# Optimization experiments

Hardware: AMD Instinct MI355X
Metric: run time of the kernel (lower is better)

## Reference

```python
import jax, jax.numpy as jnp
import numpy as np

N_NODES = 500_000
N_EDGES = 8_000_000
N_GRAPHS = 512
N_FEATURES = 128
HIDDEN = 128
N_FILT = 8
OUT_DIM = 64
BN_EPS = 1e-5


def setup_inputs() -> dict:
    key = jax.random.key(0)
    ks = jax.random.split(key, 16)
    rn = lambda k, shape, s=0.05: jax.random.normal(k, shape, jnp.float32) * s
    return {
        "x": jax.random.normal(ks[0], (N_NODES, N_FEATURES), jnp.float32),
        "W1": rn(ks[1], (N_FEATURES, HIDDEN)),
        "b1": jnp.zeros((HIDDEN,), jnp.float32),
        "W2": rn(ks[2], (HIDDEN, N_FILT)),
        "b2": jnp.zeros((N_FILT,), jnp.float32),
        "W0": rn(ks[3], (2 * N_FILT, OUT_DIM)),
        "b0": jnp.zeros((OUT_DIM,), jnp.float32),
        "g1W": rn(ks[4], (OUT_DIM, OUT_DIM)),
        "g1b": jnp.zeros((OUT_DIM,), jnp.float32),
        "l1W": rn(ks[5], (OUT_DIM, OUT_DIM)),
        "g2W": rn(ks[6], (OUT_DIM, N_FEATURES)),
        "g2b": jnp.zeros((N_FEATURES,), jnp.float32),
        "l2W": rn(ks[7], (OUT_DIM, N_FEATURES)),
        "bn_gamma": jnp.ones((N_FEATURES,), jnp.float32),
        "bn_beta": jnp.zeros((N_FEATURES,), jnp.float32),
        "edge_index": jax.random.randint(ks[8], (2, N_EDGES), 0, N_NODES),
        "batch": jnp.sort(jax.random.randint(ks[9], (N_NODES,), 0, N_GRAPHS)),
        "death_edge_idx": jax.random.randint(ks[10], (N_NODES,), 0, N_EDGES),
    }


def _deepset(x, batch, GW, Gb, LW):
    # scatter-mean over graphs, Linear (no bias), gather-broadcast subtract
    sums = jax.ops.segment_sum(x, batch, num_segments=N_GRAPHS)  # [G, d]
    cnt = jax.ops.segment_sum(jnp.ones((x.shape[0], 1), x.dtype), batch,
                              num_segments=N_GRAPHS)             # [G, 1]
    xm = (sums / jnp.maximum(cnt, 1.0)) @ LW                      # Lambda
    return x @ GW + Gb - xm[batch]                                # Gamma - gather


def reference(x, W1, b1, W2, b2, W0, b0, g1W, g1b, l1W, g2W, g2b, l2W,
              bn_gamma, bn_beta, edge_index, batch, death_edge_idx):
    # filtrations MLP: [N, F] -> [N, n_filtrations]
    filtered_v = jax.nn.relu(x @ W1 + b1) @ W2 + b2
    # edge filtration = max of endpoint values (gather + max), [E, n_filtrations]
    filtered_e = jnp.maximum(filtered_v[edge_index[0]], filtered_v[edge_index[1]])
    # persistence pairs (lower-star 0-dim generators): birth = vertex value,
    # death = paired edge value; layout [N, n_filt, 2] -> [N, 2*n_filt]
    births = filtered_v
    deaths = filtered_e[death_edge_idx]
    x0 = jnp.stack([births, deaths], axis=-1).reshape(x.shape[0], 2 * N_FILT)
    # set_fn: Linear -> ReLU -> DeepSet -> ReLU -> DeepSet
    x0 = jax.nn.relu(x0 @ W0 + b0)
    x0 = jax.nn.relu(_deepset(x0, batch, g1W, g1b, l1W))
    x0 = _deepset(x0, batch, g2W, g2b, l2W)
    # residual: x + BatchNorm1d(relu(x0)) with batch statistics
    h = jax.nn.relu(x0)
    mu = h.mean(axis=0)
    var = h.var(axis=0)
    hn = (h - mu) * jax.lax.rsqrt(var + BN_EPS)
    return x + hn * bn_gamma + bn_beta
```

## Files before the change

kernel.cpp:

```cpp
#include <hip/hip_runtime.h>
#include <hip/hip_bf16.h>

#define NNODES 500000
#define NEDGES 8000000
#define NGRAPHS 512
#define NFEAT 128
#define NHID 128
#define NFILT 8
#define ODIM 64
#define BN_EPS 1e-5f
#define NBLK2 3907
#define NBLK3 7813
#define NBLK4 977

typedef __attribute__((ext_vector_type(8))) short bf16x8;
typedef __attribute__((ext_vector_type(4))) float f32x4;
#define MFMA16(a, b, c) __builtin_amdgcn_mfma_f32_16x16x32_bf16(a, b, c, 0, 0, 0)

__device__ inline ushort f2bs(float f) {
  union { __hip_bfloat16 h; ushort u; } cv;
  cv.h = __float2bfloat16(f);
  return cv.u;
}

__global__ void k_pack(const float* __restrict__ g1W, const float* __restrict__ g2W,
                       const float* __restrict__ W1, const float* __restrict__ W0,
                       const int* __restrict__ batch,
                       ushort* __restrict__ pW1, ushort* __restrict__ pW2,
                       ushort* __restrict__ pW0, ushort* __restrict__ pW0p,
                       int* __restrict__ cnt) {
  int idx = blockIdx.x * 256 + threadIdx.x;
  if (idx < 4096) {
    int j = idx & 7, l = (idx >> 3) & 63, kb = (idx >> 9) & 1, ncb = idx >> 10;
    int k = kb * 32 + (l >> 4) * 8 + j, c = ncb * 16 + (l & 15);
    pW1[idx] = f2bs(g1W[k * 64 + c]);
  }
  if (idx < 8192) {
    int j = idx & 7, l = (idx >> 3) & 63, kb = (idx >> 9) & 1, ncb = idx >> 10;
    int k = kb * 32 + (l >> 4) * 8 + j, c = ncb * 16 + (l & 15);
    pW2[idx] = f2bs(g2W[k * 128 + c]);
  }
  if (idx < 16384) {
    int j = idx & 7, l = (idx >> 3) & 63, kb = (idx >> 9) & 3, ncb = idx >> 11;
    int k = kb * 32 + (l >> 4) * 8 + j, c = ncb * 16 + (l & 15);
    pW0[idx] = f2bs(W1[k * 128 + c]);
  }
  if (idx < 4096) {
    int j = idx & 7, l = (idx >> 3) & 63, ncb = idx >> 9;
    int k = (l >> 4) * 8 + j, c = ncb * 16 + (l & 15);
    pW0p[idx] = (k < 16) ? f2bs(W0[k * 64 + c]) : (ushort)0;
  }
  if (idx < NGRAPHS) {
    int g = idx;
    int lo0 = 0, hi0 = NNODES;
    while (lo0 < hi0) { int mid = (lo0 + hi0) >> 1; if (batch[mid] < g) lo0 = mid + 1; else hi0 = mid; }
    int lo1 = lo0, hi1 = NNODES;
    while (lo1 < hi1) { int mid = (lo1 + hi1) >> 1; if (batch[mid] < g + 1) lo1 = mid + 1; else hi1 = mid; }
    cnt[g] = lo1 - lo0;
  }
}

__global__ __launch_bounds__(256) void k_filt(
    const float* __restrict__ x, const ushort* __restrict__ pW0,
    const float* __restrict__ b1, const float* __restrict__ W2,
    const float* __restrict__ b2, ushort* __restrict__ fv16) {
  __shared__ float w2s[128 * 12];
  const int t = threadIdx.x;
  for (int i = t; i < 1024; i += 256) {
    int c = i >> 3, f = i & 7;
    w2s[c * 12 + f] = W2[i];
  }
  __syncthreads();
  const int wv = t >> 6, l = t & 63;
  const int lr = l & 15, lg = l >> 4;
  const int n0 = blockIdx.x * 128 + wv * 32;
  if (n0 >= NNODES) return;

  union { uint4 u; bf16x8 b; } bf[2][4];
#pragma unroll
  for (int mt = 0; mt < 2; ++mt)
#pragma unroll
    for (int kb = 0; kb < 4; ++kb) {
      const float* src = &x[(size_t)(n0 + mt * 16 + lr) * 128 + kb * 32 + lg * 8];
      float v[8];
      *(float4*)&v[0] = *(const float4*)src;
      *(float4*)&v[4] = *(const float4*)(src + 4);
      ushort s[8];
#pragma unroll
      for (int e = 0; e < 8; ++e) s[e] = f2bs(v[e]);
      bf[mt][kb].u = *(uint4*)s;
    }

  float pf0[8], pf1[8];
#pragma unroll
  for (int f = 0; f < 8; ++f) { pf0[f] = 0.f; pf1[f] = 0.f; }

#pragma unroll
  for (int ncb = 0; ncb < 8; ++ncb) {
    union { uint4 u; bf16x8 b; } af[4];
#pragma unroll
    for (int kb = 0; kb < 4; ++kb)
      af[kb].u = *(const uint4*)&pW0[((ncb * 4 + kb) * 64 + l) * 8];
    f32x4 a0 = (f32x4){0.f, 0.f, 0.f, 0.f};
    f32x4 a1 = (f32x4){0.f, 0.f, 0.f, 0.f};
#pragma unroll
    for (int kb = 0; kb < 4; ++kb) {
      a0 = MFMA16(af[kb].b, bf[0][kb].b, a0);
      a1 = MFMA16(af[kb].b, bf[1][kb].b, a1);
    }
    float bbv[4];
    *(float4*)bbv = *(const float4*)&b1[ncb * 16 + lg * 4];
#pragma unroll
    for (int r = 0; r < 4; ++r) {
      const int c = ncb * 16 + lg * 4 + r;
      float h0 = fmaxf(a0[r] + bbv[r], 0.f);
      float h1 = fmaxf(a1[r] + bbv[r], 0.f);
      float w20[4], w21[4];
      *(float4*)w20 = *(const float4*)&w2s[c * 12];
      *(float4*)w21 = *(const float4*)&w2s[c * 12 + 4];
#pragma unroll
      for (int f = 0; f < 4; ++f) {
        pf0[f]     = fmaf(h0, w20[f], pf0[f]);
        pf0[f + 4] = fmaf(h0, w21[f], pf0[f + 4]);
        pf1[f]     = fmaf(h1, w20[f], pf1[f]);
        pf1[f + 4] = fmaf(h1, w21[f], pf1[f + 4]);
      }
    }
  }
#pragma unroll
  for (int f = 0; f < 8; ++f) {
    pf0[f] += __shfl_xor(pf0[f], 16); pf0[f] += __shfl_xor(pf0[f], 32);
    pf1[f] += __shfl_xor(pf1[f], 16); pf1[f] += __shfl_xor(pf1[f], 32);
  }
  if (lg == 0) {
    ushort s0[8], s1[8];
#pragma unroll
    for (int f = 0; f < 8; ++f) {
      float bb = b2[f];
      s0[f] = f2bs(pf0[f] + bb);
      s1[f] = f2bs(pf1[f] + bb);
    }
    *(uint4*)&fv16[(size_t)(n0 + lr) * 8]      = *(uint4*)s0;
    *(uint4*)&fv16[(size_t)(n0 + 16 + lr) * 8] = *(uint4*)s1;
  }
}

__global__ __launch_bounds__(256) void k_pairs(
    const ushort* __restrict__ fv16, const int* __restrict__ edge_index,
    const int* __restrict__ didx, const int* __restrict__ batch,
    const ushort* __restrict__ pW0p, const float* __restrict__ b0,
    ushort* __restrict__ y, float* __restrict__ sums1) {
  __shared__ float ps[4][64];
  __shared__ int pg[4];
  const int t = threadIdx.x, wv = t >> 6, l = t & 63;
  const int lr = l & 15, lg = l >> 4, c0 = lg * 4;
  const int nbase = blockIdx.x * 512;

  union { uint4 u; bf16x8 b; } af[4];
#pragma unroll
  for (int ncb = 0; ncb < 4; ++ncb)
    af[ncb].u = *(const uint4*)&pW0p[(ncb * 64 + l) * 8];

  for (int tile = 0; tile < 4; ++tile) {
    const int n0 = nbase + tile * 128 + wv * 32;
    if (n0 < NNODES) {
      union { uint4 u; bf16x8 b; } bf[2];
      int gN[2];
#pragma unroll
      for (int mt = 0; mt < 2; ++mt) {
        const int n = n0 + mt * 16 + lr;
        gN[mt] = batch[n];
        bf[mt].u = make_uint4(0u, 0u, 0u, 0u);
        if (lg < 2) {
          const int de = didx[n];
          const int u = edge_index[de];
          const int v = edge_index[NEDGES + de];
          ushort4 bb = *(const ushort4*)&fv16[(size_t)n * 8 + lg * 4];
          ushort4 ub = *(const ushort4*)&fv16[(size_t)u * 8 + lg * 4];
          ushort4 vb = *(const ushort4*)&fv16[(size_t)v * 8 + lg * 4];
          const ushort* bp = (const ushort*)&bb;
          const ushort* up = (const ushort*)&ub;
          const ushort* vp = (const ushort*)&vb;
          ushort s[8];
#pragma unroll
          for (int j = 0; j < 4; ++j) {
            s[2 * j] = bp[j];
            float uf = __uint_as_float((unsigned)up[j] << 16);
            float vf = __uint_as_float((unsigned)vp[j] << 16);
            s[2 * j + 1] = (uf > vf) ? up[j] : vp[j];
          }
          bf[mt].u = *(uint4*)s;
        }
      }

      f32x4 acc[2][4];
#pragma unroll
      for (int mt = 0; mt < 2; ++mt)
#pragma unroll
        for (int ncb = 0; ncb < 4; ++ncb) {
          acc[mt][ncb] = (f32x4){0.f, 0.f, 0.f, 0.f};
          acc[mt][ncb] = MFMA16(af[ncb].b, bf[mt].b, acc[mt][ncb]);
        }

      const int g_first = __shfl(gN[0], 0);
      float wsum[4][4];
#pragma unroll
      for (int ncb = 0; ncb < 4; ++ncb)
#pragma unroll
        for (int r = 0; r < 4; ++r) wsum[ncb][r] = 0.f;

#pragma unroll
      for (int mt = 0; mt < 2; ++mt) {
        const int n = n0 + mt * 16 + lr;
        const int g = gN[mt];
        const bool prim = (g == g_first);
#pragma unroll
        for (int ncb = 0; ncb < 4; ++ncb) {
          const int c = ncb * 16 + c0;
          float bbv[4];
          *(float4*)bbv = *(const float4*)&b0[c];
          ushort st[4];
#pragma unroll
          for (int r = 0; r < 4; ++r) {
            float v = fmaxf(acc[mt][ncb][r] + bbv[r], 0.f);
            st[r] = f2bs(v);
            if (prim) wsum[ncb][r] += v;
            else atomicAdd(&sums1[g * 64 + c + r], v);
          }
          *(ushort4*)&y[(size_t)n * 64 + c] = *(ushort4*)st;
        }
      }
#pragma unroll
      for (int ncb = 0; ncb < 4; ++ncb)
#pragma unroll
        for (int r = 0; r < 4; ++r) {
          float w = wsum[ncb][r];
          w += __shfl_xor(w, 1); w += __shfl_xor(w, 2);
          w += __shfl_xor(w, 4); w += __shfl_xor(w, 8);
          if (lr == 0) ps[wv][ncb * 16 + c0 + r] = w;
        }
      if (l == 0) pg[wv] = g_first;
    } else {
      ps[wv][l] = 0.f;
      if (l == 0) pg[wv] = -1;
    }
    __syncthreads();

    if (t < 64) {
      const int bg = pg[0];
      float s = 0.f;
#pragma unroll
      for (int w = 0; w < 4; ++w) {
        const int gv = pg[w];
        if (gv < 0) continue;
        if (gv == bg) s += ps[w][t];
        else atomicAdd(&sums1[gv * 64 + t], ps[w][t]);
      }
      if (bg >= 0) atomicAdd(&sums1[bg * 64 + t], s);
    }
    __syncthreads();
  }
}

template <int D>
__global__ void k_meanlin(const float* __restrict__ sums,
                          const int* __restrict__ cnt,
                          const float* __restrict__ LW,
                          float* __restrict__ xm) {
  __shared__ float m[64];
  const int g = blockIdx.x, t = threadIdx.x;
  const float c = fmaxf((float)cnt[g], 1.f);
  if (t < 64) m[t] = sums[g * 64 + t] / c;
  __syncthreads();
  float a = 0.f;
#pragma unroll
  for (int k = 0; k < 64; ++k) a = fmaf(m[k], LW[k * D + t], a);
  xm[g * D + t] = a;
}

__global__ __launch_bounds__(256) void k_ds1(
    const ushort* __restrict__ ybf, const int* __restrict__ batch,
    const ushort* __restrict__ pW1, const float* __restrict__ g1b,
    const float* __restrict__ xm1, ushort* __restrict__ y2,
    float* __restrict__ sums2) {
  __shared__ float ps[4][64];
  __shared__ int pg[4];
  const int t = threadIdx.x, wv = t >> 6, l = t & 63;
  const int lr = l & 15, lg = l >> 4, c0 = lg * 4;
  const int nbase = blockIdx.x * 512;

  union { uint4 u; bf16x8 b; } af[4][2];
#pragma unroll
  for (int ncb = 0; ncb < 4; ++ncb)
#pragma unroll
    for (int kb = 0; kb < 2; ++kb)
      af[ncb][kb].u = *(const uint4*)&pW1[((ncb * 2 + kb) * 64 + l) * 8];

  for (int tile = 0; tile < 4; ++tile) {
    const int n0 = nbase + tile * 128 + wv * 32;
    if (n0 < NNODES) {
      union { uint4 u; bf16x8 b; } bf[2][2];
#pragma unroll
      for (int mt = 0; mt < 2; ++mt)
#pragma unroll
        for (int kb = 0; kb < 2; ++kb)
          bf[mt][kb].u = *(const uint4*)&ybf[(size_t)(n0 + mt * 16 + lr) * 64 + kb * 32 + lg * 8];

      f32x4 acc[2][4];
#pragma unroll
      for (int mt = 0; mt < 2; ++mt)
#pragma unroll
        for (int ncb = 0; ncb < 4; ++ncb) {
          acc[mt][ncb] = (f32x4){0.f, 0.f, 0.f, 0.f};
          acc[mt][ncb] = MFMA16(af[ncb][0].b, bf[mt][0].b, acc[mt][ncb]);
          acc[mt][ncb] = MFMA16(af[ncb][1].b, bf[mt][1].b, acc[mt][ncb]);
        }

      const int g0 = batch[n0 + lr], g1 = batch[n0 + 16 + lr];
      const int g_first = __shfl(g0, 0);

      float wsum[4][4];
#pragma unroll
      for (int ncb = 0; ncb < 4; ++ncb)
#pragma unroll
        for (int r = 0; r < 4; ++r) wsum[ncb][r] = 0.f;

#pragma unroll
      for (int mt = 0; mt < 2; ++mt) {
        const int n = n0 + mt * 16 + lr;
        const int g = mt ? g1 : g0;
        const bool prim = (g == g_first);
#pragma unroll
        for (int ncb = 0; ncb < 4; ++ncb) {
          const int c = ncb * 16 + c0;
          float xmv[4], bbv[4];
          *(float4*)xmv = *(const float4*)&xm1[g * 64 + c];
          *(float4*)bbv = *(const float4*)&g1b[c];
          ushort st[4];
#pragma unroll
          for (int r = 0; r < 4; ++r) {
            float v = fmaxf(acc[mt][ncb][r] + bbv[r] - xmv[r], 0.f);
            st[r] = f2bs(v);
            if (prim) wsum[ncb][r] += v;
            else atomicAdd(&sums2[g * 64 + c + r], v);
          }
          *(ushort4*)&y2[(size_t)n * 64 + c] = *(ushort4*)st;
        }
      }
#pragma unroll
      for (int ncb = 0; ncb < 4; ++ncb)
#pragma unroll
        for (int r = 0; r < 4; ++r) {
          float w = wsum[ncb][r];
          w += __shfl_xor(w, 1); w += __shfl_xor(w, 2);
          w += __shfl_xor(w, 4); w += __shfl_xor(w, 8);
          if (lr == 0) ps[wv][ncb * 16 + c0 + r] = w;
        }
      if (l == 0) pg[wv] = g_first;
    } else {
      ps[wv][l] = 0.f;
      if (l == 0) pg[wv] = -1;
    }
    __syncthreads();

    if (t < 64) {
      const int bg = pg[0];
      float s = 0.f;
#pragma unroll
      for (int w = 0; w < 4; ++w) {
        const int gv = pg[w];
        if (gv < 0) continue;
        if (gv == bg) s += ps[w][t];
        else atomicAdd(&sums2[gv * 64 + t], ps[w][t]);
      }
      if (bg >= 0) atomicAdd(&sums2[bg * 64 + t], s);
    }
    __syncthreads();
  }
}

__global__ __launch_bounds__(256) void k_ds2a(
    const ushort* __restrict__ y2, const int* __restrict__ batch,
    const ushort* __restrict__ pW2, const float* __restrict__ g2b,
    const float* __restrict__ xm2,
    float* __restrict__ pmu, float* __restrict__ psq) {
  __shared__ float ps[4][128], pq[4][128];
  const int t = threadIdx.x, wv = t >> 6, l = t & 63;
  const int lr = l & 15, lg = l >> 4, c0 = lg * 4;
  const int nbase = blockIdx.x * 512;

  float sw[8][4], sq[8][4];
#pragma unroll
  for (int ncb = 0; ncb < 8; ++ncb)
#pragma unroll
    for (int r = 0; r < 4; ++r) { sw[ncb][r] = 0.f; sq[ncb][r] = 0.f; }

  for (int tile = 0; tile < 4; ++tile) {
    const int n0 = nbase + tile * 128 + wv * 32;
    if (n0 >= NNODES) continue;

    union { uint4 u; bf16x8 b; } bf[2][2];
#pragma unroll
    for (int mt = 0; mt < 2; ++mt)
#pragma unroll
      for (int kb = 0; kb < 2; ++kb)
        bf[mt][kb].u = *(const uint4*)&y2[(size_t)(n0 + mt * 16 + lr) * 64 + kb * 32 + lg * 8];

    const int g0 = batch[n0 + lr], g1 = batch[n0 + 16 + lr];

#pragma unroll
    for (int ncb = 0; ncb < 8; ++ncb) {
      union { uint4 u; bf16x8 b; } af0, af1;
      af0.u = *(const uint4*)&pW2[((ncb * 2 + 0) * 64 + l) * 8];
      af1.u = *(const uint4*)&pW2[((ncb * 2 + 1) * 64 + l) * 8];
      f32x4 a0 = (f32x4){0.f, 0.f, 0.f, 0.f}, a1 = (f32x4){0.f, 0.f, 0.f, 0.f};
      a0 = MFMA16(af0.b, bf[0][0].b, a0); a0 = MFMA16(af1.b, bf[0][1].b, a0);
      a1 = MFMA16(af0.b, bf[1][0].b, a1); a1 = MFMA16(af1.b, bf[1][1].b, a1);

      const int c = ncb * 16 + c0;
      float xm0[4], xm1v[4], bbv[4];
      *(float4*)xm0 = *(const float4*)&xm2[g0 * 128 + c];
      *(float4*)xm1v = *(const float4*)&xm2[g1 * 128 + c];
      *(float4*)bbv = *(const float4*)&g2b[c];
#pragma unroll
      for (int r = 0; r < 4; ++r) {
        float v0 = fmaxf(a0[r] + bbv[r] - xm0[r], 0.f);
        float v1 = fmaxf(a1[r] + bbv[r] - xm1v[r], 0.f);
        sw[ncb][r] += v0 + v1;
        sq[ncb][r] = fmaf(v0, v0, fmaf(v1, v1, sq[ncb][r]));
      }
    }
  }

#pragma unroll
  for (int ncb = 0; ncb < 8; ++ncb)
#pragma unroll
    for (int r = 0; r < 4; ++r) {
      float wr = sw[ncb][r], qr = sq[ncb][r];
      wr += __shfl_xor(wr, 1); wr += __shfl_xor(wr, 2);
      wr += __shfl_xor(wr, 4); wr += __shfl_xor(wr, 8);
      qr += __shfl_xor(qr, 1); qr += __shfl_xor(qr, 2);
      qr += __shfl_xor(qr, 4); qr += __shfl_xor(qr, 8);
      if (lr == 0) { ps[wv][ncb * 16 + c0 + r] = wr; pq[wv][ncb * 16 + c0 + r] = qr; }
    }
  __syncthreads();
  if (t < 128) {
    pmu[(size_t)blockIdx.x * 128 + t] = ps[0][t] + ps[1][t] + ps[2][t] + ps[3][t];
    psq[(size_t)blockIdx.x * 128 + t] = pq[0][t] + pq[1][t] + pq[2][t] + pq[3][t];
  }
}

__global__ void k_red(const float* __restrict__ pmu, const float* __restrict__ psq,
                      float* __restrict__ musum, float* __restrict__ sqsum) {
  const int f = threadIdx.x & 127;
  const bool mu = threadIdx.x < 128;
  const float* src = mu ? pmu : psq;
  float s = 0.f;
  for (int b = blockIdx.x; b < NBLK4; b += 32) s += src[(size_t)b * 128 + f];
  atomicAdd(mu ? &musum[f] : &sqsum[f], s);
}

__global__ __launch_bounds__(256) void k_bn(
    const ushort* __restrict__ y2, const int* __restrict__ batch,
    const ushort* __restrict__ pW2, const float* __restrict__ g2b,
    const float* __restrict__ xm2, const float* __restrict__ x,
    const float* __restrict__ musum, const float* __restrict__ sqsum,
    const float* __restrict__ gamma, const float* __restrict__ beta,
    float* __restrict__ out) {
  __shared__ float vs[64 * 132];
  __shared__ float smu[128], ssc[128], sbe[128];
  const int t = threadIdx.x, wv = t >> 6, l = t & 63;
  const int lr = l & 15, lg = l >> 4, c0 = lg * 4;
  if (t < 128) {
    const float invN = 1.f / (float)NNODES;
    float m = musum[t] * invN;
    float v = sqsum[t] * invN - m * m;
    smu[t] = m;
    ssc[t] = rsqrtf(v + BN_EPS) * gamma[t];
    sbe[t] = beta[t];
  }
  const int nblk = blockIdx.x * 64;
  const int n0 = nblk + wv * 16;

  if (n0 < NNODES) {
    union { uint4 u; bf16x8 b; } bf[2];
#pragma unroll
    for (int kb = 0; kb < 2; ++kb)
      bf[kb].u = *(const uint4*)&y2[(size_t)(n0 + lr) * 64 + kb * 32 + lg * 8];

    const int g0 = batch[n0 + lr];
    const int row0 = wv * 16 + lr;

#pragma unroll
    for (int ncb = 0; ncb < 8; ++ncb) {
      union { uint4 u; bf16x8 b; } af0, af1;
      af0.u = *(const uint4*)&pW2[((ncb * 2 + 0) * 64 + l) * 8];
      af1.u = *(const uint4*)&pW2[((ncb * 2 + 1) * 64 + l) * 8];
      f32x4 a0 = (f32x4){0.f, 0.f, 0.f, 0.f};
      a0 = MFMA16(af0.b, bf[0].b, a0);
      a0 = MFMA16(af1.b, bf[1].b, a0);

      const int c = ncb * 16 + c0;
      float bbv[4], xm0[4], hvv[4];
      *(float4*)bbv = *(const float4*)&g2b[c];
      *(float4*)xm0 = *(const float4*)&xm2[g0 * 128 + c];
#pragma unroll
      for (int r = 0; r < 4; ++r)
        hvv[r] = fmaxf(a0[r] + bbv[r] - xm0[r], 0.f);
      *(float4*)&vs[row0 * 132 + c] = *(float4*)hvv;
    }
  }
  __syncthreads();

  const int rmax = NNODES - nblk;
  for (int i = t; i < 2048; i += 256) {
    const int row = i >> 5, c4 = (i & 31) * 4;
    if (row >= rmax) break;
    const int n = nblk + row;
    float hv[4], muv[4], scv[4], bev[4], xv[4], o[4];
    *(float4*)hv = *(const float4*)&vs[row * 132 + c4];
    *(float4*)muv = *(const float4*)&smu[c4];
    *(float4*)scv = *(const float4*)&ssc[c4];
    *(float4*)bev = *(const float4*)&sbe[c4];
    *(float4*)xv = *(const float4*)&x[(size_t)n * 128 + c4];
#pragma unroll
    for (int r = 0; r < 4; ++r)
      o[r] = xv[r] + (hv[r] - muv[r]) * scv[r] + bev[r];
    *(float4*)&out[(size_t)n * 128 + c4] = *(float4*)o;
  }
}

extern "C" void kernel_launch(void* const* d_in, const int* in_sizes, int n_in,
                              void* d_out, int out_size, void* d_ws,
                              size_t ws_size, hipStream_t stream) {
  const float* x     = (const float*)d_in[0];
  const float* W1    = (const float*)d_in[1];
  const float* b1    = (const float*)d_in[2];
  const float* W2    = (const float*)d_in[3];
  const float* b2    = (const float*)d_in[4];
  const float* W0    = (const float*)d_in[5];
  const float* b0    = (const float*)d_in[6];
  const float* g1W   = (const float*)d_in[7];
  const float* g1b   = (const float*)d_in[8];
  const float* l1W   = (const float*)d_in[9];
  const float* g2W   = (const float*)d_in[10];
  const float* g2b   = (const float*)d_in[11];
  const float* l2W   = (const float*)d_in[12];
  const float* gamma = (const float*)d_in[13];
  const float* beta  = (const float*)d_in[14];
  const int* edge_index = (const int*)d_in[15];
  const int* batch      = (const int*)d_in[16];
  const int* didx       = (const int*)d_in[17];
  float* out = (float*)d_out;

  char* ws = (char*)d_ws;
  ushort* fv16  = (ushort*)(ws + 0);
  float*  pmu   = (float*) (ws + 0);
  float*  psq   = (float*) (ws + 2000384);
  ushort* ybf   = (ushort*)(ws + 16000000);
  ushort* y2    = (ushort*)(ws + 80000000);
  float*  sums1 = (float*) (ws + 144000000);
  float*  sums2 = (float*) (ws + 144131072);
  float*  musum = (float*) (ws + 144262144);
  float*  sqsum = (float*) (ws + 144262656);
  int*    cnt   = (int*)   (ws + 144263168);
  float*  xm1   = (float*) (ws + 144265216);
  float*  xm2   = (float*) (ws + 144396288);
  ushort* pW1   = (ushort*)(ws + 144658432);
  ushort* pW2   = (ushort*)(ws + 144666624);
  ushort* pW0   = (ushort*)(ws + 144683008);
  ushort* pW0p  = (ushort*)(ws + 144715776);

  hipMemsetAsync(ws + 144000000, 0, 263168, stream);

  k_pack<<<64, 256, 0, stream>>>(g1W, g2W, W1, W0, batch, pW1, pW2, pW0, pW0p, cnt);
  k_filt<<<NBLK2, 256, 0, stream>>>(x, pW0, b1, W2, b2, fv16);
  k_pairs<<<NBLK4, 256, 0, stream>>>(fv16, edge_index, didx, batch, pW0p, b0, ybf, sums1);
  k_meanlin<64><<<NGRAPHS, 64, 0, stream>>>(sums1, cnt, l1W, xm1);
  k_ds1<<<NBLK4, 256, 0, stream>>>(ybf, batch, pW1, g1b, xm1, y2, sums2);
  k_meanlin<128><<<NGRAPHS, 128, 0, stream>>>(sums2, cnt, l2W, xm2);
  k_ds2a<<<NBLK4, 256, 0, stream>>>(y2, batch, pW2, g2b, xm2, pmu, psq);
  k_red<<<32, 256, 0, stream>>>(pmu, psq, musum, sqsum);
  k_bn<<<NBLK3, 256, 0, stream>>>(y2, batch, pW2, g2b, xm2, x, musum, sqsum,
                                  gamma, beta, out);
}
```

Before: 523.4 us.

## Prefetch gather indices and next tiles; replace block-level segment reduction with per-wave flush

Result: slower. 623.6 us (+19.2%).

```diff
diff --git a/kernel.cpp b/kernel.cpp
--- a/kernel.cpp
+++ b/kernel.cpp
@@ -150,116 +150,119 @@
     const int* __restrict__ didx, const int* __restrict__ batch,
     const ushort* __restrict__ pW0p, const float* __restrict__ b0,
     ushort* __restrict__ y, float* __restrict__ sums1) {
-  __shared__ float ps[4][64];
-  __shared__ int pg[4];
   const int t = threadIdx.x, wv = t >> 6, l = t & 63;
   const int lr = l & 15, lg = l >> 4, c0 = lg * 4;
   const int nbase = blockIdx.x * 512;
 
-  union { uint4 u; bf16x8 b; } af[4];
+  union U { uint4 u; bf16x8 b; };
+  U af[4];
 #pragma unroll
   for (int ncb = 0; ncb < 4; ++ncb)
     af[ncb].u = *(const uint4*)&pW0p[(ncb * 64 + l) * 8];
 
+  int de[4][2];
+#pragma unroll
+  for (int tile = 0; tile < 4; ++tile)
+#pragma unroll
+    for (int mt = 0; mt < 2; ++mt) {
+      const int n = nbase + tile * 128 + wv * 32 + mt * 16 + lr;
+      de[tile][mt] = (lg < 2 && n < NNODES) ? didx[n] : 0;
+    }
+  int uu[4][2], vvx[4][2];
+#pragma unroll
+  for (int tile = 0; tile < 4; ++tile)
+#pragma unroll
+    for (int mt = 0; mt < 2; ++mt) {
+      const int n = nbase + tile * 128 + wv * 32 + mt * 16 + lr;
+      if (lg < 2 && n < NNODES) {
+        uu[tile][mt]  = edge_index[de[tile][mt]];
+        vvx[tile][mt] = edge_index[NEDGES + de[tile][mt]];
+      } else { uu[tile][mt] = 0; vvx[tile][mt] = 0; }
+    }
+
+  float wsum[4][4];
+#pragma unroll
+  for (int ncb = 0; ncb < 4; ++ncb)
+#pragma unroll
+    for (int r = 0; r < 4; ++r) wsum[ncb][r] = 0.f;
+  int cur_g = -1;
+
+#define FLUSH_P() do { if (cur_g >= 0) {                                  \
+    for (int ncb_ = 0; ncb_ < 4; ++ncb_)                                  \
+      for (int r_ = 0; r_ < 4; ++r_) {                                    \
+        float w_ = wsum[ncb_][r_];                                        \
+        w_ += __shfl_xor(w_, 1); w_ += __shfl_xor(w_, 2);                 \
+        w_ += __shfl_xor(w_, 4); w_ += __shfl_xor(w_, 8);                 \
+        if (lr == 0) atomicAdd(&sums1[cur_g * 64 + ncb_ * 16 + c0 + r_], w_); \
+        wsum[ncb_][r_] = 0.f;                                             \
+      } } } while (0)
+
   for (int tile = 0; tile < 4; ++tile) {
     const int n0 = nbase + tile * 128 + wv * 32;
-    if (n0 < NNODES) {
-      union { uint4 u; bf16x8 b; } bf[2];
-      int gN[2];
-#pragma unroll
-      for (int mt = 0; mt < 2; ++mt) {
-        const int n = n0 + mt * 16 + lr;
-        gN[mt] = batch[n];
-        bf[mt].u = make_uint4(0u, 0u, 0u, 0u);
-        if (lg < 2) {
-          const int de = didx[n];
-          const int u = edge_index[de];
-          const int v = edge_index[NEDGES + de];
-          ushort4 bb = *(const ushort4*)&fv16[(size_t)n * 8 + lg * 4];
-          ushort4 ub = *(const ushort4*)&fv16[(size_t)u * 8 + lg * 4];
-          ushort4 vb = *(const ushort4*)&fv16[(size_t)v * 8 + lg * 4];
-          const ushort* bp = (const ushort*)&bb;
-          const ushort* up = (const ushort*)&ub;
-          const ushort* vp = (const ushort*)&vb;
-          ushort s[8];
-#pragma unroll
-          for (int j = 0; j < 4; ++j) {
-            s[2 * j] = bp[j];
-            float uf = __uint_as_float((unsigned)up[j] << 16);
-            float vf = __uint_as_float((unsigned)vp[j] << 16);
-            s[2 * j + 1] = (uf > vf) ? up[j] : vp[j];
-          }
-          bf[mt].u = *(uint4*)s;
+    if (n0 >= NNODES) break;
+
+    U bf[2];
+    int gN[2];
+#pragma unroll
+    for (int mt = 0; mt < 2; ++mt) {
+      const int n = n0 + mt * 16 + lr;
+      gN[mt] = batch[n];
+      bf[mt].u = make_uint4(0u, 0u, 0u, 0u);
+      if (lg < 2) {
+        ushort4 bb = *(const ushort4*)&fv16[(size_t)n * 8 + lg * 4];
+        ushort4 ub = *(const ushort4*)&fv16[(size_t)uu[tile][mt] * 8 + lg * 4];
+        ushort4 vb = *(const ushort4*)&fv16[(size_t)vvx[tile][mt] * 8 + lg * 4];
+        const ushort* bp = (const ushort*)&bb;
+        const ushort* up = (const ushort*)&ub;
+        const ushort* vp = (const ushort*)&vb;
+        ushort s[8];
+#pragma unroll
+        for (int j = 0; j < 4; ++j) {
+          s[2 * j] = bp[j];
+          float uf = __uint_as_float((unsigned)up[j] << 16);
+          float vf = __uint_as_float((unsigned)vp[j] << 16);
+          s[2 * j + 1] = (uf > vf) ? up[j] : vp[j];
         }
+        bf[mt].u = *(uint4*)s;
       }
-
-      f32x4 acc[2][4];
-#pragma unroll
-      for (int mt = 0; mt < 2; ++mt)
-#pragma unroll
-        for (int ncb = 0; ncb < 4; ++ncb) {
-          acc[mt][ncb] = (f32x4){0.f, 0.f, 0.f, 0.f};
-          acc[mt][ncb] = MFMA16(af[ncb].b, bf[mt].b, acc[mt][ncb]);
+    }
+
+    f32x4 acc[2][4];
+#pragma unroll
+    for (int mt = 0; mt < 2; ++mt)
+#pragma unroll
+      for (int ncb = 0; ncb < 4; ++ncb) {
+        acc[mt][ncb] = (f32x4){0.f, 0.f, 0.f, 0.f};
+        acc[mt][ncb] = MFMA16(af[ncb].b, bf[mt].b, acc[mt][ncb]);
+      }
+
+    const int g_first = __shfl(gN[0], 0);
+    const bool uni = __all(gN[0] == g_first) && __all(gN[1] == g_first);
+    if (uni && g_first != cur_g) { FLUSH_P(); cur_g = g_first; }
+
+#pragma unroll
+    for (int mt = 0; mt < 2; ++mt) {
+      const int n = n0 + mt * 16 + lr;
+      const int g = gN[mt];
+#pragma unroll
+      for (int ncb = 0; ncb < 4; ++ncb) {
+        const int c = ncb * 16 + c0;
+        float bbv[4];
+        *(float4*)bbv = *(const float4*)&b0[c];
+        ushort st[4];
+#pragma unroll
+        for (int r = 0; r < 4; ++r) {
+          float v = fmaxf(acc[mt][ncb][r] + bbv[r], 0.f);
+          st[r] = f2bs(v);
+          if (uni) wsum[ncb][r] += v;
+          else atomicAdd(&sums1[g * 64 + c + r], v);
         }
-
-      const int g_first = __shfl(gN[0], 0);
-      float wsum[4][4];
-#pragma unroll
-      for (int ncb = 0; ncb < 4; ++ncb)
-#pragma unroll
-        for (int r = 0; r < 4; ++r) wsum[ncb][r] = 0.f;
-
-#pragma unroll
-      for (int mt = 0; mt < 2; ++mt) {
-        const int n = n0 + mt * 16 + lr;
-        const int g = gN[mt];
-        const bool prim = (g == g_first);
-#pragma unroll
-        for (int ncb = 0; ncb < 4; ++ncb) {
-          const int c = ncb * 16 + c0;
-          float bbv[4];
-          *(float4*)bbv = *(const float4*)&b0[c];
-          ushort st[4];
-#pragma unroll
-          for (int r = 0; r < 4; ++r) {
-            float v = fmaxf(acc[mt][ncb][r] + bbv[r], 0.f);
-            st[r] = f2bs(v);
-            if (prim) wsum[ncb][r] += v;
-            else atomicAdd(&sums1[g * 64 + c + r], v);
-          }
-          *(ushort4*)&y[(size_t)n * 64 + c] = *(ushort4*)st;
-        }
+        *(ushort4*)&y[(size_t)n * 64 + c] = *(ushort4*)st;
       }
-#pragma unroll
-      for (int ncb = 0; ncb < 4; ++ncb)
-#pragma unroll
-        for (int r = 0; r < 4; ++r) {
-          float w = wsum[ncb][r];
-          w += __shfl_xor(w, 1); w += __shfl_xor(w, 2);
-          w += __shfl_xor(w, 4); w += __shfl_xor(w, 8);
-          if (lr == 0) ps[wv][ncb * 16 + c0 + r] = w;
-        }
-      if (l == 0) pg[wv] = g_first;
-    } else {
-      ps[wv][l] = 0.f;
-      if (l == 0) pg[wv] = -1;
-    }
-    __syncthreads();
-
-    if (t < 64) {
-      const int bg = pg[0];
-      float s = 0.f;
-#pragma unroll
-      for (int w = 0; w < 4; ++w) {
-        const int gv = pg[w];
-        if (gv < 0) continue;
-        if (gv == bg) s += ps[w][t];
-        else atomicAdd(&sums1[gv * 64 + t], ps[w][t]);
-      }
-      if (bg >= 0) atomicAdd(&sums1[bg * 64 + t], s);
-    }
-    __syncthreads();
-  }
+    }
+  }
+  FLUSH_P();
+#undef FLUSH_P
 }
 
 template <int D>
@@ -283,100 +286,98 @@
     const ushort* __restrict__ pW1, const float* __restrict__ g1b,
     const float* __restrict__ xm1, ushort* __restrict__ y2,
     float* __restrict__ sums2) {
-  __shared__ float ps[4][64];
-  __shared__ int pg[4];
   const int t = threadIdx.x, wv = t >> 6, l = t & 63;
   const int lr = l & 15, lg = l >> 4, c0 = lg * 4;
   const int nbase = blockIdx.x * 512;
 
-  union { uint4 u; bf16x8 b; } af[4][2];
+  union U { uint4 u; bf16x8 b; };
+  U af[4][2];
 #pragma unroll
   for (int ncb = 0; ncb < 4; ++ncb)
 #pragma unroll
     for (int kb = 0; kb < 2; ++kb)
       af[ncb][kb].u = *(const uint4*)&pW1[((ncb * 2 + kb) * 64 + l) * 8];
 
+  float wsum[4][4];
+#pragma unroll
+  for (int ncb = 0; ncb < 4; ++ncb)
+#pragma unroll
+    for (int r = 0; r < 4; ++r) wsum[ncb][r] = 0.f;
+  int cur_g = -1;
+
+#define FLUSH_D() do { if (cur_g >= 0) {                                  \
+    for (int ncb_ = 0; ncb_ < 4; ++ncb_)                                  \
+      for (int r_ = 0; r_ < 4; ++r_) {                                    \
+        float w_ = wsum[ncb_][r_];                                        \
+        w_ += __shfl_xor(w_, 1); w_ += __shfl_xor(w_, 2);                 \
+        w_ += __shfl_xor(w_, 4); w_ += __shfl_xor(w_, 8);                 \
+        if (lr == 0) atomicAdd(&sums2[cur_g * 64 + ncb_ * 16 + c0 + r_], w_); \
+        wsum[ncb_][r_] = 0.f;                                             \
+      } } } while (0)
+
+  U bfP[2][2], bfQ[2][2];
+  {
+    const int n0 = nbase + wv * 32;
+    if (n0 < NNODES)
+#pragma unroll
+      for (int mt = 0; mt < 2; ++mt)
+#pragma unroll
+        for (int kb = 0; kb < 2; ++kb)
+          bfP[mt][kb].u = *(const uint4*)&ybf[(size_t)(n0 + mt * 16 + lr) * 64 + kb * 32 + lg * 8];
+  }
+
   for (int tile = 0; tile < 4; ++tile) {
     const int n0 = nbase + tile * 128 + wv * 32;
-    if (n0 < NNODES) {
-      union { uint4 u; bf16x8 b; } bf[2][2];
+    if (n0 >= NNODES) break;
+    U (*cur)[2] = (tile & 1) ? bfQ : bfP;
+    U (*nxt)[2] = (tile & 1) ? bfP : bfQ;
+    const int n1 = n0 + 128;
+    if (tile < 3 && n1 < NNODES)
 #pragma unroll
       for (int mt = 0; mt < 2; ++mt)
 #pragma unroll
         for (int kb = 0; kb < 2; ++kb)
-          bf[mt][kb].u = *(const uint4*)&ybf[(size_t)(n0 + mt * 16 + lr) * 64 + kb * 32 + lg * 8];
-
-      f32x4 acc[2][4];
-#pragma unroll
-      for (int mt = 0; mt < 2; ++mt)
-#pragma unroll
-        for (int ncb = 0; ncb < 4; ++ncb) {
-          acc[mt][ncb] = (f32x4){0.f, 0.f, 0.f, 0.f};
-          acc[mt][ncb] = MFMA16(af[ncb][0].b, bf[mt][0].b, acc[mt][ncb]);
-          acc[mt][ncb] = MFMA16(af[ncb][1].b, bf[mt][1].b, acc[mt][ncb]);
+          nxt[mt][kb].u = *(const uint4*)&ybf[(size_t)(n1 + mt * 16 + lr) * 64 + kb * 32 + lg * 8];
+
+    f32x4 acc[2][4];
+#pragma unroll
+    for (int mt = 0; mt < 2; ++mt)
+#pragma unroll
+      for (int ncb = 0; ncb < 4; ++ncb) {
+        acc[mt][ncb] = (f32x4){0.f, 0.f, 0.f, 0.f};
+        acc[mt][ncb] = MFMA16(af[ncb][0].b, cur[mt][0].b, acc[mt][ncb]);
+        acc[mt][ncb] = MFMA16(af[ncb][1].b, cur[mt][1].b, acc[mt][ncb]);
+      }
+
+    const int g0 = batch[n0 + lr], g1 = batch[n0 + 16 + lr];
+    const int g_first = __shfl(g0, 0);
+    const bool uni = __all(g0 == g_first) && __all(g1 == g_first);
+    if (uni && g_first != cur_g) { FLUSH_D(); cur_g = g_first; }
+
+#pragma unroll
+    for (int mt = 0; mt < 2; ++mt) {
+      const int n = n0 + mt * 16 + lr;
+      const int g = mt ? g1 : g0;
+#pragma unroll
+      for (int ncb = 0; ncb < 4; ++ncb) {
+        const int c = ncb * 16 + c0;
+        float xmv[4], bbv[4];
+        *(float4*)xmv = *(const float4*)&xm1[g * 64 + c];
+        *(float4*)bbv = *(const float4*)&g1b[c];
+        ushort st[4];
+#pragma unroll
+        for (int r = 0; r < 4; ++r) {
+          float v = fmaxf(acc[mt][ncb][r] + bbv[r] - xmv[r], 0.f);
+          st[r] = f2bs(v);
+          if (uni) wsum[ncb][r] += v;
+          else atomicAdd(&sums2[g * 64 + c + r], v);
         }
-
-      const int g0 = batch[n0 + lr], g1 = batch[n0 + 16 + lr];
-      const int g_first = __shfl(g0, 0);
-
-      float wsum[4][4];
-#pragma unroll
-      for (int ncb = 0; ncb < 4; ++ncb)
-#pragma unroll
-        for (int r = 0; r < 4; ++r) wsum[ncb][r] = 0.f;
-
-#pragma unroll
-      for (int mt = 0; mt < 2; ++mt) {
-        const int n = n0 + mt * 16 + lr;
-        const int g = mt ? g1 : g0;
-        const bool prim = (g == g_first);
-#pragma unroll
-        for (int ncb = 0; ncb < 4; ++ncb) {
-          const int c = ncb * 16 + c0;
-          float xmv[4], bbv[4];
-          *(float4*)xmv = *(const float4*)&xm1[g * 64 + c];
-          *(float4*)bbv = *(const float4*)&g1b[c];
-          ushort st[4];
-#pragma unroll
-          for (int r = 0; r < 4; ++r) {
-            float v = fmaxf(acc[mt][ncb][r] + bbv[r] - xmv[r], 0.f);
-            st[r] = f2bs(v);
-            if (prim) wsum[ncb][r] += v;
-            else atomicAdd(&sums2[g * 64 + c + r], v);
-          }
-          *(ushort4*)&y2[(size_t)n * 64 + c] = *(ushort4*)st;
-        }
+        *(ushort4*)&y2[(size_t)n * 64 + c] = *(ushort4*)st;
       }
-#pragma unroll
-      for (int ncb = 0; ncb < 4; ++ncb)
-#pragma unroll
-        for (int r = 0; r < 4; ++r) {
-          float w = wsum[ncb][r];
-          w += __shfl_xor(w, 1); w += __shfl_xor(w, 2);
-          w += __shfl_xor(w, 4); w += __shfl_xor(w, 8);
-          if (lr == 0) ps[wv][ncb * 16 + c0 + r] = w;
-        }
-      if (l == 0) pg[wv] = g_first;
-    } else {
-      ps[wv][l] = 0.f;
-      if (l == 0) pg[wv] = -1;
-    }
-    __syncthreads();
-
-    if (t < 64) {
-      const int bg = pg[0];
-      float s = 0.f;
-#pragma unroll
-      for (int w = 0; w < 4; ++w) {
-        const int gv = pg[w];
-        if (gv < 0) continue;
-        if (gv == bg) s += ps[w][t];
-        else atomicAdd(&sums2[gv * 64 + t], ps[w][t]);
-      }
-      if (bg >= 0) atomicAdd(&sums2[bg * 64 + t], s);
-    }
-    __syncthreads();
-  }
+    }
+  }
+  FLUSH_D();
+#undef FLUSH_D
 }
 
 __global__ __launch_bounds__(256) void k_ds2a(
@@ -389,33 +390,48 @@
   const int lr = l & 15, lg = l >> 4, c0 = lg * 4;
   const int nbase = blockIdx.x * 512;
 
+  union U { uint4 u; bf16x8 b; };
   float sw[8][4], sq[8][4];
 #pragma unroll
   for (int ncb = 0; ncb < 8; ++ncb)
 #pragma unroll
     for (int r = 0; r < 4; ++r) { sw[ncb][r] = 0.f; sq[ncb][r] = 0.f; }
+
+  U bfP[2][2], bfQ[2][2];
+  {
+    const int n0 = nbase + wv * 32;
+    if (n0 < NNODES)
+#pragma unroll
+      for (int mt = 0; mt < 2; ++mt)
+#pragma unroll
+        for (int kb = 0; kb < 2; ++kb)
+          bfP[mt][kb].u = *(const uint4*)&y2[(size_t)(n0 + mt * 16 + lr) * 64 + kb * 32 + lg * 8];
+  }
 
   for (int tile = 0; tile < 4; ++tile) {
     const int n0 = nbase + tile * 128 + wv * 32;
-    if (n0 >= NNODES) continue;
-
-    union { uint4 u; bf16x8 b; } bf[2][2];
-#pragma unroll
-    for (int mt = 0; mt < 2; ++mt)
-#pragma unroll
-      for (int kb = 0; kb < 2; ++kb)
-        bf[mt][kb].u = *(const uint4*)&y2[(size_t)(n0 + mt * 16 + lr) * 64 + kb * 32 + lg * 8];
+    const bool act = n0 < NNODES;
+    U (*cur)[2] = (tile & 1) ? bfQ : bfP;
+    U (*nxt)[2] = (tile & 1) ? bfP : bfQ;
+    const int n1 = n0 + 128;
+    if (tile < 3 && n1 < NNODES)
+#pragma unroll
+      for (int mt = 0; mt < 2; ++mt)
+#pragma unroll
+        for (int kb = 0; kb < 2; ++kb)
+          nxt[mt][kb].u = *(const uint4*)&y2[(size_t)(n1 + mt * 16 + lr) * 64 + kb * 32 + lg * 8];
+    if (!act) continue;
 
     const int g0 = batch[n0 + lr], g1 = batch[n0 + 16 + lr];
 
 #pragma unroll
     for (int ncb = 0; ncb < 8; ++ncb) {
-      union { uint4 u; bf16x8 b; } af0, af1;
+      U af0, af1;
       af0.u = *(const uint4*)&pW2[((ncb * 2 + 0) * 64 + l) * 8];
       af1.u = *(const uint4*)&pW2[((ncb * 2 + 1) * 64 + l) * 8];
       f32x4 a0 = (f32x4){0.f, 0.f, 0.f, 0.f}, a1 = (f32x4){0.f, 0.f, 0.f, 0.f};
-      a0 = MFMA16(af0.b, bf[0][0].b, a0); a0 = MFMA16(af1.b, bf[0][1].b, a0);
-      a1 = MFMA16(af0.b, bf[1][0].b, a1); a1 = MFMA16(af1.b, bf[1][1].b, a1);
+      a0 = MFMA16(af0.b, cur[0][0].b, a0); a0 = MFMA16(af1.b, cur[0][1].b, a0);
+      a1 = MFMA16(af0.b, cur[1][0].b, a1); a1 = MFMA16(af1.b, cur[1][1].b, a1);
 
       const int c = ncb * 16 + c0;
       float xm0[4], xm1v[4], bbv[4];
```
